# Kernel optimization log

Hardware: AMD Instinct MI355X
Metric: run time of the kernel (lower is better)

## Reference

```python
import jax, jax.numpy as jnp
import numpy as np

B, H, S, DK = 4, 16, 2048, 64
NEG_INF = -1e9


def setup_inputs() -> dict:
    key = jax.random.key(0)
    kq, kk, kv, ks = jax.random.split(key, 4)
    q = jax.random.normal(kq, (B, H, S, DK), dtype=jnp.float32)
    k = jax.random.normal(kk, (B, H, S, DK), dtype=jnp.float32)
    v = jax.random.normal(kv, (B, H, S, DK), dtype=jnp.float32)
    # valid lengths in [S//2, S] so no row is fully masked (causal + padding)
    sen_len = jax.random.randint(ks, (B,), S // 2, S + 1, dtype=jnp.int64)
    return {"q": q, "k": k, "v": v, "sen_len": sen_len}


def reference(q, k, v, sen_len):
    # att = q @ k^T / sqrt(d_k)   -> (B, H, S, S)
    att = jnp.einsum("bhqd,bhkd->bhqk", q, k) / np.sqrt(DK).astype(np.float32)
    pos = jnp.arange(S)
    # causal (ahead) mask: query i may not attend to key j > i
    causal = pos[None, :] > pos[:, None]                      # (S, S)
    # padding mask: key positions >= sen_len[b] are invalid
    pad = pos[None, :] >= sen_len[:, None]                    # (B, S)
    mask = causal[None, None, :, :] | pad[:, None, None, :]   # (B, 1, S, S) broadcast over H
    att = jnp.where(mask, jnp.float32(NEG_INF), att)
    att = jax.nn.softmax(att, axis=-1)
    return jnp.einsum("bhqk,bhkd->bhqd", att, v)
```

## Files before the change

### kernel.cpp

```cpp
#include <hip/hip_runtime.h>
#include <hip/hip_bf16.h>

#define B_   4
#define H_   16
#define S_   2048
#define DK_  64
#define NBH  64
#define QSCALE (0.125f * 1.44269504f)

typedef __attribute__((ext_vector_type(8)))  short    short8;
typedef __attribute__((ext_vector_type(4)))  float    f32x4;
typedef __attribute__((ext_vector_type(16))) float    f32x16;
typedef __attribute__((ext_vector_type(4)))  unsigned u32x4;

__device__ __forceinline__ unsigned short f2bf(float f) {
    union { float f; unsigned int u; } x; x.f = f;
    unsigned int r = x.u + 0x7fffu + ((x.u >> 16) & 1u);
    return (unsigned short)(r >> 16);
}

__device__ __forceinline__ unsigned cvtpk(float a, float b) {
    unsigned r;
    asm("v_cvt_pk_bf16_f32 %0, %1, %2" : "=v"(r) : "v"(a), "v"(b));
    return r;
}
__device__ __forceinline__ void pl32swap(unsigned& a, unsigned& b) {
    asm("v_permlane32_swap_b32 %0, %1" : "+v"(a), "+v"(b));
}

__global__ __launch_bounds__(256) void conv_k(const float* __restrict__ in,
                                              unsigned short* __restrict__ out) {
    const long i = (long)(blockIdx.x * 256 + threadIdx.x) * 8;
    const float4* p = (const float4*)(in + i);
    float4 a = p[0], b = p[1];
    short8 f;
    f[0] = (short)f2bf(a.x); f[1] = (short)f2bf(a.y);
    f[2] = (short)f2bf(a.z); f[3] = (short)f2bf(a.w);
    f[4] = (short)f2bf(b.x); f[5] = (short)f2bf(b.y);
    f[6] = (short)f2bf(b.z); f[7] = (short)f2bf(b.w);
    *(short8*)(out + i) = f;
}

__global__ __launch_bounds__(256) void transp_v(const float* __restrict__ v,
                                                unsigned short* __restrict__ vt) {
    const int s0 = blockIdx.x * 64;
    const int bh = blockIdx.y;
    const int s  = threadIdx.x & 63;
    const int dq = threadIdx.x >> 6;
    const float* src = v + ((long)bh * S_ + s0 + s) * DK_;
    unsigned short* dst = vt + (long)bh * DK_ * S_ + s0 + s;
    #pragma unroll
    for (int j4 = 0; j4 < 4; ++j4) {
        const int d4 = dq * 16 + j4 * 4;
        float4 a = *(const float4*)(src + d4);
        dst[(long)(d4 + 0) * S_] = f2bf(a.x);
        dst[(long)(d4 + 1) * S_] = f2bf(a.y);
        dst[(long)(d4 + 2) * S_] = f2bf(a.z);
        dst[(long)(d4 + 3) * S_] = f2bf(a.w);
    }
}

template <bool PRECONV>
__global__ __launch_bounds__(256, 2) void attn_fwd3(
    const float* __restrict__ q, const float* __restrict__ k32,
    const float* __restrict__ v32, const unsigned short* __restrict__ kbf,
    const unsigned short* __restrict__ vtbf, const int* __restrict__ sen_len,
    float* __restrict__ out)
{
    const int qt = (S_ / 128 - 1) - blockIdx.x;
    const int bh = blockIdx.y;
    const int b  = bh >> 4;
    const int q0 = qt * 128;
    const long base = (long)bh * S_ * DK_;

    const int tid  = threadIdx.x;
    const int wid  = tid >> 6;
    const int lane = tid & 63;
    const int l31  = lane & 31;
    const int hi   = lane >> 5;

    __shared__ unsigned short Klds[64 * 64];
    __shared__ unsigned short Vlds[64 * 64];
    char* const KldsB = (char*)Klds;
    char* const VldsB = (char*)Vlds;

    const int slen = sen_len[b];
    const int q0w  = q0 + wid * 32;
    const int iq   = q0w + l31;

    short8 qf[4];
    {
        const float* qp = q + base + (long)iq * DK_ + hi * 8;
        #pragma unroll
        for (int ks = 0; ks < 4; ++ks) {
            float4 a = *(const float4*)(qp + ks * 16);
            float4 c = *(const float4*)(qp + ks * 16 + 4);
            short8 f;
            f[0] = (short)f2bf(a.x * QSCALE); f[1] = (short)f2bf(a.y * QSCALE);
            f[2] = (short)f2bf(a.z * QSCALE); f[3] = (short)f2bf(a.w * QSCALE);
            f[4] = (short)f2bf(c.x * QSCALE); f[5] = (short)f2bf(c.y * QSCALE);
            f[6] = (short)f2bf(c.z * QSCALE); f[7] = (short)f2bf(c.w * QSCALE);
            qf[ks] = f;
        }
    }

    f32x16 O0 = (f32x16)(0.f), O1 = (f32x16)(0.f);
    float m_ = -INFINITY, l_ = 0.f;

    const int nk     = min(q0 + 128, slen);
    const int ntiles = (nk + 63) >> 6;
    const int wmax   = q0w + 31;

    for (int t = 0; t < ntiles; ++t) {
        const int k0 = t * 64;

        if (PRECONV) {
            const unsigned short* ksrc = kbf + base + (long)k0 * DK_;
            const unsigned short* vsrc = vtbf + (long)bh * DK_ * S_ + k0;
            #pragma unroll
            for (int it = 0; it < 2; ++it) {
                const int c = tid + 256 * it;
                const int r = c >> 3, slot = c & 7;
                const int dst = r * 128 + ((slot * 16) ^ ((r & 7) << 4));
                *(short8*)(KldsB + dst) = *(const short8*)(ksrc + r * DK_ + slot * 8);
                *(short8*)(VldsB + dst) = *(const short8*)(vsrc + (long)r * S_ + slot * 8);
            }
        } else {
            const float* ks32 = k32 + base + (long)k0 * DK_;
            #pragma unroll
            for (int it = 0; it < 2; ++it) {
                const int c = tid + 256 * it;
                const int r = c >> 3, slot = c & 7;
                const float4* p = (const float4*)(ks32 + r * DK_ + slot * 8);
                float4 a = p[0], bq = p[1];
                short8 f;
                f[0] = (short)f2bf(a.x);  f[1] = (short)f2bf(a.y);
                f[2] = (short)f2bf(a.z);  f[3] = (short)f2bf(a.w);
                f[4] = (short)f2bf(bq.x); f[5] = (short)f2bf(bq.y);
                f[6] = (short)f2bf(bq.z); f[7] = (short)f2bf(bq.w);
                *(short8*)(KldsB + r * 128 + ((slot * 16) ^ ((r & 7) << 4))) = f;
            }
            const float* vs32 = v32 + base + (long)k0 * DK_;
            #pragma unroll
            for (int it = 0; it < 4; ++it) {
                const int c = tid + 256 * it;
                const int s = c >> 4, d4 = (c & 15) * 4;
                float4 a = *(const float4*)(vs32 + s * DK_ + d4);
                unsigned short vals[4] = {f2bf(a.x), f2bf(a.y), f2bf(a.z), f2bf(a.w)};
                #pragma unroll
                for (int j = 0; j < 4; ++j)
                    *(unsigned short*)(VldsB + (d4 + j) * 128 +
                                       ((2 * s) ^ (((d4 + j) & 7) << 4))) = vals[j];
            }
        }
        __syncthreads();

        if (k0 <= wmax) {
            f32x16 s0 = (f32x16)(0.f), s1 = (f32x16)(0.f);
            #pragma unroll
            for (int ks = 0; ks < 4; ++ks) {
                const int col = ks * 32 + hi * 16;
                const int r0 = l31, r1 = 32 + l31;
                short8 kf0 = *(const short8*)(KldsB + r0 * 128 + (col ^ ((r0 & 7) << 4)));
                short8 kf1 = *(const short8*)(KldsB + r1 * 128 + (col ^ ((r1 & 7) << 4)));
                s0 = __builtin_amdgcn_mfma_f32_32x32x16_bf16(kf0, qf[ks], s0, 0, 0, 0);
                s1 = __builtin_amdgcn_mfma_f32_32x32x16_bf16(kf1, qf[ks], s1, 0, 0, 0);
            }

            if (!((k0 + 63 <= q0w) && (k0 + 63 < slen))) {
                #pragma unroll
                for (int r = 0; r < 16; ++r) {
                    const int joff = k0 + (r & 3) + 8 * (r >> 2) + 4 * hi;
                    const int j0 = joff, j1 = joff + 32;
                    if (!((j0 <= iq) && (j0 < slen))) s0[r] = -1e30f;
                    if (!((j1 <= iq) && (j1 < slen))) s1[r] = -1e30f;
                }
            }

            float pm = s0[0];
            #pragma unroll
            for (int r = 1; r < 16; ++r) pm = fmaxf(pm, s0[r]);
            #pragma unroll
            for (int r = 0; r < 16; ++r) pm = fmaxf(pm, s1[r]);
            pm = fmaxf(pm, __shfl_xor(pm, 32, 64));
            const float mnew = fmaxf(m_, pm);
            const float resc = exp2f(m_ - mnew);
            m_ = mnew;
            float rs = 0.f;
            #pragma unroll
            for (int r = 0; r < 16; ++r) { s0[r] = exp2f(s0[r] - mnew); rs += s0[r]; }
            #pragma unroll
            for (int r = 0; r < 16; ++r) { s1[r] = exp2f(s1[r] - mnew); rs += s1[r]; }
            rs += __shfl_xor(rs, 32, 64);
            l_ = l_ * resc + rs;
            O0 *= resc;
            O1 *= resc;

            u32x4 pw[4];
            {
                unsigned a0 = cvtpk(s0[0], s0[1]),  c0 = cvtpk(s0[2], s0[3]);
                unsigned b0 = cvtpk(s0[4], s0[5]),  d0 = cvtpk(s0[6], s0[7]);
                pl32swap(a0, b0); pl32swap(c0, d0);
                pw[0] = (u32x4){a0, c0, b0, d0};
                unsigned a1 = cvtpk(s0[8], s0[9]),  c1 = cvtpk(s0[10], s0[11]);
                unsigned b1 = cvtpk(s0[12], s0[13]), d1 = cvtpk(s0[14], s0[15]);
                pl32swap(a1, b1); pl32swap(c1, d1);
                pw[1] = (u32x4){a1, c1, b1, d1};
                unsigned a2 = cvtpk(s1[0], s1[1]),  c2 = cvtpk(s1[2], s1[3]);
                unsigned b2 = cvtpk(s1[4], s1[5]),  d2 = cvtpk(s1[6], s1[7]);
                pl32swap(a2, b2); pl32swap(c2, d2);
                pw[2] = (u32x4){a2, c2, b2, d2};
                unsigned a3 = cvtpk(s1[8], s1[9]),  c3 = cvtpk(s1[10], s1[11]);
                unsigned b3 = cvtpk(s1[12], s1[13]), d3 = cvtpk(s1[14], s1[15]);
                pl32swap(a3, b3); pl32swap(c3, d3);
                pw[3] = (u32x4){a3, c3, b3, d3};
            }

            #pragma unroll
            for (int s = 0; s < 4; ++s) {
                short8 pf = __builtin_bit_cast(short8, pw[s]);
                const int col = s * 32 + hi * 16;
                const int r0 = l31, r1 = 32 + l31;
                short8 vf0 = *(const short8*)(VldsB + r0 * 128 + (col ^ ((r0 & 7) << 4)));
                short8 vf1 = *(const short8*)(VldsB + r1 * 128 + (col ^ ((r1 & 7) << 4)));
                O0 = __builtin_amdgcn_mfma_f32_32x32x16_bf16(vf0, pf, O0, 0, 0, 0);
                O1 = __builtin_amdgcn_mfma_f32_32x32x16_bf16(vf1, pf, O1, 0, 0, 0);
            }
        }
        __syncthreads();
    }

    const float inv = 1.0f / l_;
    float* op = out + base + (long)iq * DK_;
    #pragma unroll
    for (int rq = 0; rq < 4; ++rq) {
        float4 f0, f1;
        f0.x = O0[rq * 4 + 0] * inv; f0.y = O0[rq * 4 + 1] * inv;
        f0.z = O0[rq * 4 + 2] * inv; f0.w = O0[rq * 4 + 3] * inv;
        f1.x = O1[rq * 4 + 0] * inv; f1.y = O1[rq * 4 + 1] * inv;
        f1.z = O1[rq * 4 + 2] * inv; f1.w = O1[rq * 4 + 3] * inv;
        *(float4*)(op + rq * 8 + hi * 4)      = f0;
        *(float4*)(op + 32 + rq * 8 + hi * 4) = f1;
    }
}

extern "C" void kernel_launch(void* const* d_in, const int* in_sizes, int n_in,
                              void* d_out, int out_size, void* d_ws, size_t ws_size,
                              hipStream_t stream) {
    const float* q = (const float*)d_in[0];
    const float* k = (const float*)d_in[1];
    const float* v = (const float*)d_in[2];
    const int* sen_len = (const int*)d_in[3];
    float* out = (float*)d_out;

    const size_t kv_elems = (size_t)NBH * S_ * DK_;
    const bool pre = ws_size >= kv_elems * 2 * sizeof(unsigned short);
    unsigned short* kbf  = (unsigned short*)d_ws;
    unsigned short* vtbf = kbf + kv_elems;

    if (pre) {
        conv_k<<<dim3((unsigned)(kv_elems / 2048)), dim3(256), 0, stream>>>(k, kbf);
        transp_v<<<dim3(S_ / 64, NBH), dim3(256), 0, stream>>>(v, vtbf);
        attn_fwd3<true><<<dim3(S_ / 128, NBH), dim3(256), 0, stream>>>(
            q, k, v, kbf, vtbf, sen_len, out);
    } else {
        attn_fwd3<false><<<dim3(S_ / 128, NBH), dim3(256), 0, stream>>>(
            q, k, v, kbf, vtbf, sen_len, out);
    }
}
```

Measured before the change: 229.7 us.

## Double-buffer K/V tiles in LDS with register prefetch and lazy softmax rescale

K/V tiles now live in two LDS buffers. The next tile is loaded into registers before the current tile's MFMA work and written to the other buffer afterwards, which leaves one barrier per tile instead of two. The change also raises the launch-bounds occupancy hint to 4 blocks, adds s_setprio around the MFMA sections, and uses a tree max reduction. The running max is now rescaled only when the new max exceeds the old by more than 8, which skips most O rescales. The costs are higher register pressure from the prefetch registers under a tighter register budget, plus a slightly different numeric path for the softmax.

Result: slower. 238.2 us (+3.7%).

```diff
diff --git a/kernel.cpp b/kernel.cpp
--- a/kernel.cpp
+++ b/kernel.cpp
@@ -9,7 +9,6 @@
 #define QSCALE (0.125f * 1.44269504f)
 
 typedef __attribute__((ext_vector_type(8)))  short    short8;
-typedef __attribute__((ext_vector_type(4)))  float    f32x4;
 typedef __attribute__((ext_vector_type(16))) float    f32x16;
 typedef __attribute__((ext_vector_type(4)))  unsigned u32x4;
 
@@ -18,7 +17,6 @@
     unsigned int r = x.u + 0x7fffu + ((x.u >> 16) & 1u);
     return (unsigned short)(r >> 16);
 }
-
 __device__ __forceinline__ unsigned cvtpk(float a, float b) {
     unsigned r;
     asm("v_cvt_pk_bf16_f32 %0, %1, %2" : "=v"(r) : "v"(a), "v"(b));
@@ -61,7 +59,7 @@
 }
 
 template <bool PRECONV>
-__global__ __launch_bounds__(256, 2) void attn_fwd3(
+__global__ __launch_bounds__(256, 4) void attn_fwd4(
     const float* __restrict__ q, const float* __restrict__ k32,
     const float* __restrict__ v32, const unsigned short* __restrict__ kbf,
     const unsigned short* __restrict__ vtbf, const int* __restrict__ sen_len,
@@ -71,7 +69,8 @@
     const int bh = blockIdx.y;
     const int b  = bh >> 4;
     const int q0 = qt * 128;
-    const long base = (long)bh * S_ * DK_;
+    const long base   = (long)bh * S_ * DK_;
+    const long vtbase = (long)bh * DK_ * S_;
 
     const int tid  = threadIdx.x;
     const int wid  = tid >> 6;
@@ -79,10 +78,8 @@
     const int l31  = lane & 31;
     const int hi   = lane >> 5;
 
-    __shared__ unsigned short Klds[64 * 64];
-    __shared__ unsigned short Vlds[64 * 64];
-    char* const KldsB = (char*)Klds;
-    char* const VldsB = (char*)Vlds;
+    __shared__ unsigned short Klds[2][64 * 64];
+    __shared__ unsigned short Vlds[2][64 * 64];
 
     const int slen = sen_len[b];
     const int q0w  = q0 + wid * 32;
@@ -111,90 +108,130 @@
     const int ntiles = (nk + 63) >> 6;
     const int wmax   = q0w + 31;
 
+    if (PRECONV) {
+        const unsigned short* ksrc = kbf + base;
+        const unsigned short* vsrc = vtbf + vtbase;
+        #pragma unroll
+        for (int it = 0; it < 2; ++it) {
+            const int c = tid + 256 * it, r = c >> 3, slot = c & 7;
+            const int dst = r * 128 + ((slot * 16) ^ ((r & 7) << 4));
+            *(short8*)((char*)Klds[0] + dst) = *(const short8*)(ksrc + r * DK_ + slot * 8);
+            *(short8*)((char*)Vlds[0] + dst) = *(const short8*)(vsrc + (long)r * S_ + slot * 8);
+        }
+    } else {
+        const float* ks32 = k32 + base;
+        #pragma unroll
+        for (int it = 0; it < 2; ++it) {
+            const int c = tid + 256 * it, r = c >> 3, slot = c & 7;
+            const float4* p = (const float4*)(ks32 + r * DK_ + slot * 8);
+            float4 a = p[0], bq = p[1];
+            short8 f;
+            f[0] = (short)f2bf(a.x);  f[1] = (short)f2bf(a.y);
+            f[2] = (short)f2bf(a.z);  f[3] = (short)f2bf(a.w);
+            f[4] = (short)f2bf(bq.x); f[5] = (short)f2bf(bq.y);
+            f[6] = (short)f2bf(bq.z); f[7] = (short)f2bf(bq.w);
+            *(short8*)((char*)Klds[0] + r * 128 + ((slot * 16) ^ ((r & 7) << 4))) = f;
+        }
+        const float* vs32 = v32 + base;
+        #pragma unroll
+        for (int it = 0; it < 4; ++it) {
+            const int c = tid + 256 * it, s = c >> 4, d4 = (c & 15) * 4;
+            float4 a = *(const float4*)(vs32 + s * DK_ + d4);
+            unsigned short vals[4] = {f2bf(a.x), f2bf(a.y), f2bf(a.z), f2bf(a.w)};
+            #pragma unroll
+            for (int j = 0; j < 4; ++j)
+                *(unsigned short*)((char*)Vlds[0] + (d4 + j) * 128 +
+                                   ((2 * s) ^ (((d4 + j) & 7) << 4))) = vals[j];
+        }
+    }
+    __syncthreads();
+
+    int cur = 0;
     for (int t = 0; t < ntiles; ++t) {
         const int k0 = t * 64;
-
-        if (PRECONV) {
-            const unsigned short* ksrc = kbf + base + (long)k0 * DK_;
-            const unsigned short* vsrc = vtbf + (long)bh * DK_ * S_ + k0;
-            #pragma unroll
-            for (int it = 0; it < 2; ++it) {
-                const int c = tid + 256 * it;
-                const int r = c >> 3, slot = c & 7;
-                const int dst = r * 128 + ((slot * 16) ^ ((r & 7) << 4));
-                *(short8*)(KldsB + dst) = *(const short8*)(ksrc + r * DK_ + slot * 8);
-                *(short8*)(VldsB + dst) = *(const short8*)(vsrc + (long)r * S_ + slot * 8);
-            }
-        } else {
-            const float* ks32 = k32 + base + (long)k0 * DK_;
-            #pragma unroll
-            for (int it = 0; it < 2; ++it) {
-                const int c = tid + 256 * it;
-                const int r = c >> 3, slot = c & 7;
-                const float4* p = (const float4*)(ks32 + r * DK_ + slot * 8);
-                float4 a = p[0], bq = p[1];
-                short8 f;
-                f[0] = (short)f2bf(a.x);  f[1] = (short)f2bf(a.y);
-                f[2] = (short)f2bf(a.z);  f[3] = (short)f2bf(a.w);
-                f[4] = (short)f2bf(bq.x); f[5] = (short)f2bf(bq.y);
-                f[6] = (short)f2bf(bq.z); f[7] = (short)f2bf(bq.w);
-                *(short8*)(KldsB + r * 128 + ((slot * 16) ^ ((r & 7) << 4))) = f;
-            }
-            const float* vs32 = v32 + base + (long)k0 * DK_;
-            #pragma unroll
-            for (int it = 0; it < 4; ++it) {
-                const int c = tid + 256 * it;
-                const int s = c >> 4, d4 = (c & 15) * 4;
-                float4 a = *(const float4*)(vs32 + s * DK_ + d4);
-                unsigned short vals[4] = {f2bf(a.x), f2bf(a.y), f2bf(a.z), f2bf(a.w)};
-                #pragma unroll
-                for (int j = 0; j < 4; ++j)
-                    *(unsigned short*)(VldsB + (d4 + j) * 128 +
-                                       ((2 * s) ^ (((d4 + j) & 7) << 4))) = vals[j];
-            }
-        }
-        __syncthreads();
+        const bool more = (t + 1 < ntiles);
+
+        short8 kst[2], vst[2];
+        float4 kr[2][2], vr[4];
+        if (more) {
+            if (PRECONV) {
+                const unsigned short* ksrc = kbf + base + (long)(k0 + 64) * DK_;
+                const unsigned short* vsrc = vtbf + vtbase + (k0 + 64);
+                #pragma unroll
+                for (int it = 0; it < 2; ++it) {
+                    const int c = tid + 256 * it, r = c >> 3, slot = c & 7;
+                    kst[it] = *(const short8*)(ksrc + r * DK_ + slot * 8);
+                    vst[it] = *(const short8*)(vsrc + (long)r * S_ + slot * 8);
+                }
+            } else {
+                const float* ks32 = k32 + base + (long)(k0 + 64) * DK_;
+                #pragma unroll
+                for (int it = 0; it < 2; ++it) {
+                    const int c = tid + 256 * it, r = c >> 3, slot = c & 7;
+                    kr[it][0] = *(const float4*)(ks32 + r * DK_ + slot * 8);
+                    kr[it][1] = *(const float4*)(ks32 + r * DK_ + slot * 8 + 4);
+                }
+                const float* vs32 = v32 + base + (long)(k0 + 64) * DK_;
+                #pragma unroll
+                for (int it = 0; it < 4; ++it) {
+                    const int c = tid + 256 * it, s = c >> 4, d4 = (c & 15) * 4;
+                    vr[it] = *(const float4*)(vs32 + s * DK_ + d4);
+                }
+            }
+        }
+        __builtin_amdgcn_sched_barrier(0);
 
         if (k0 <= wmax) {
+            const char* KB = (const char*)Klds[cur];
+            const char* VB = (const char*)Vlds[cur];
+            const int sw = (l31 & 7) << 4;
+            const int rb = l31 * 128;
+
             f32x16 s0 = (f32x16)(0.f), s1 = (f32x16)(0.f);
+            __builtin_amdgcn_s_setprio(1);
             #pragma unroll
             for (int ks = 0; ks < 4; ++ks) {
-                const int col = ks * 32 + hi * 16;
-                const int r0 = l31, r1 = 32 + l31;
-                short8 kf0 = *(const short8*)(KldsB + r0 * 128 + (col ^ ((r0 & 7) << 4)));
-                short8 kf1 = *(const short8*)(KldsB + r1 * 128 + (col ^ ((r1 & 7) << 4)));
+                const int col = (ks * 32 + hi * 16) ^ sw;
+                short8 kf0 = *(const short8*)(KB + rb + col);
+                short8 kf1 = *(const short8*)(KB + 4096 + rb + col);
                 s0 = __builtin_amdgcn_mfma_f32_32x32x16_bf16(kf0, qf[ks], s0, 0, 0, 0);
                 s1 = __builtin_amdgcn_mfma_f32_32x32x16_bf16(kf1, qf[ks], s1, 0, 0, 0);
             }
+            __builtin_amdgcn_s_setprio(0);
 
             if (!((k0 + 63 <= q0w) && (k0 + 63 < slen))) {
                 #pragma unroll
                 for (int r = 0; r < 16; ++r) {
                     const int joff = k0 + (r & 3) + 8 * (r >> 2) + 4 * hi;
-                    const int j0 = joff, j1 = joff + 32;
-                    if (!((j0 <= iq) && (j0 < slen))) s0[r] = -1e30f;
-                    if (!((j1 <= iq) && (j1 < slen))) s1[r] = -1e30f;
-                }
-            }
-
-            float pm = s0[0];
-            #pragma unroll
-            for (int r = 1; r < 16; ++r) pm = fmaxf(pm, s0[r]);
-            #pragma unroll
-            for (int r = 0; r < 16; ++r) pm = fmaxf(pm, s1[r]);
+                    if (!((joff <= iq) && (joff < slen))) s0[r] = -1e30f;
+                    if (!((joff + 32 <= iq) && (joff + 32 < slen))) s1[r] = -1e30f;
+                }
+            }
+
+            float x[16];
+            #pragma unroll
+            for (int i = 0; i < 16; ++i) x[i] = fmaxf(s0[i], s1[i]);
+            #pragma unroll
+            for (int st = 8; st >= 1; st >>= 1)
+                #pragma unroll
+                for (int i = 0; i < 8; ++i)
+                    if (i < st) x[i] = fmaxf(x[i], x[i + st]);
+            float pm = x[0];
             pm = fmaxf(pm, __shfl_xor(pm, 32, 64));
-            const float mnew = fmaxf(m_, pm);
-            const float resc = exp2f(m_ - mnew);
-            m_ = mnew;
-            float rs = 0.f;
-            #pragma unroll
-            for (int r = 0; r < 16; ++r) { s0[r] = exp2f(s0[r] - mnew); rs += s0[r]; }
-            #pragma unroll
-            for (int r = 0; r < 16; ++r) { s1[r] = exp2f(s1[r] - mnew); rs += s1[r]; }
-            rs += __shfl_xor(rs, 32, 64);
-            l_ = l_ * resc + rs;
-            O0 *= resc;
-            O1 *= resc;
+            if (!__all(pm <= m_ + 8.0f)) {
+                const float mn = fmaxf(m_, pm);
+                const float rc = exp2f(m_ - mn);
+                m_ = mn; l_ *= rc;
+                O0 *= rc; O1 *= rc;
+            }
+            float rs[4] = {0.f, 0.f, 0.f, 0.f};
+            #pragma unroll
+            for (int i = 0; i < 16; ++i) { s0[i] = exp2f(s0[i] - m_); rs[i & 3] += s0[i]; }
+            #pragma unroll
+            for (int i = 0; i < 16; ++i) { s1[i] = exp2f(s1[i] - m_); rs[i & 3] += s1[i]; }
+            float rsum = (rs[0] + rs[1]) + (rs[2] + rs[3]);
+            rsum += __shfl_xor(rsum, 32, 64);
+            l_ += rsum;
 
             u32x4 pw[4];
             {
@@ -202,7 +239,7 @@
                 unsigned b0 = cvtpk(s0[4], s0[5]),  d0 = cvtpk(s0[6], s0[7]);
                 pl32swap(a0, b0); pl32swap(c0, d0);
                 pw[0] = (u32x4){a0, c0, b0, d0};
-                unsigned a1 = cvtpk(s0[8], s0[9]),  c1 = cvtpk(s0[10], s0[11]);
+                unsigned a1 = cvtpk(s0[8], s0[9]),   c1 = cvtpk(s0[10], s0[11]);
                 unsigned b1 = cvtpk(s0[12], s0[13]), d1 = cvtpk(s0[14], s0[15]);
                 pl32swap(a1, b1); pl32swap(c1, d1);
                 pw[1] = (u32x4){a1, c1, b1, d1};
@@ -210,24 +247,63 @@
                 unsigned b2 = cvtpk(s1[4], s1[5]),  d2 = cvtpk(s1[6], s1[7]);
                 pl32swap(a2, b2); pl32swap(c2, d2);
                 pw[2] = (u32x4){a2, c2, b2, d2};
-                unsigned a3 = cvtpk(s1[8], s1[9]),  c3 = cvtpk(s1[10], s1[11]);
+                unsigned a3 = cvtpk(s1[8], s1[9]),   c3 = cvtpk(s1[10], s1[11]);
                 unsigned b3 = cvtpk(s1[12], s1[13]), d3 = cvtpk(s1[14], s1[15]);
                 pl32swap(a3, b3); pl32swap(c3, d3);
                 pw[3] = (u32x4){a3, c3, b3, d3};
             }
 
+            __builtin_amdgcn_s_setprio(1);
             #pragma unroll
             for (int s = 0; s < 4; ++s) {
                 short8 pf = __builtin_bit_cast(short8, pw[s]);
-                const int col = s * 32 + hi * 16;
-                const int r0 = l31, r1 = 32 + l31;
-                short8 vf0 = *(const short8*)(VldsB + r0 * 128 + (col ^ ((r0 & 7) << 4)));
-                short8 vf1 = *(const short8*)(VldsB + r1 * 128 + (col ^ ((r1 & 7) << 4)));
+                const int col = (s * 32 + hi * 16) ^ sw;
+                short8 vf0 = *(const short8*)(VB + rb + col);
+                short8 vf1 = *(const short8*)(VB + 4096 + rb + col);
                 O0 = __builtin_amdgcn_mfma_f32_32x32x16_bf16(vf0, pf, O0, 0, 0, 0);
                 O1 = __builtin_amdgcn_mfma_f32_32x32x16_bf16(vf1, pf, O1, 0, 0, 0);
             }
-        }
-        __syncthreads();
+            __builtin_amdgcn_s_setprio(0);
+        }
+        __builtin_amdgcn_sched_barrier(0);
+
+        if (more) {
+            char* KB = (char*)Klds[cur ^ 1];
+            char* VB = (char*)Vlds[cur ^ 1];
+            if (PRECONV) {
+                #pragma unroll
+                for (int it = 0; it < 2; ++it) {
+                    const int c = tid + 256 * it, r = c >> 3, slot = c & 7;
+                    const int dst = r * 128 + ((slot * 16) ^ ((r & 7) << 4));
+                    *(short8*)(KB + dst) = kst[it];
+                    *(short8*)(VB + dst) = vst[it];
+                }
+            } else {
+                #pragma unroll
+                for (int it = 0; it < 2; ++it) {
+                    const int c = tid + 256 * it, r = c >> 3, slot = c & 7;
+                    float4 a = kr[it][0], bq = kr[it][1];
+                    short8 f;
+                    f[0] = (short)f2bf(a.x);  f[1] = (short)f2bf(a.y);
+                    f[2] = (short)f2bf(a.z);  f[3] = (short)f2bf(a.w);
+                    f[4] = (short)f2bf(bq.x); f[5] = (short)f2bf(bq.y);
+                    f[6] = (short)f2bf(bq.z); f[7] = (short)f2bf(bq.w);
+                    *(short8*)(KB + r * 128 + ((slot * 16) ^ ((r & 7) << 4))) = f;
+                }
+                #pragma unroll
+                for (int it = 0; it < 4; ++it) {
+                    const int c = tid + 256 * it, s = c >> 4, d4 = (c & 15) * 4;
+                    float4 a = vr[it];
+                    unsigned short vals[4] = {f2bf(a.x), f2bf(a.y), f2bf(a.z), f2bf(a.w)};
+                    #pragma unroll
+                    for (int j = 0; j < 4; ++j)
+                        *(unsigned short*)(VB + (d4 + j) * 128 +
+                                           ((2 * s) ^ (((d4 + j) & 7) << 4))) = vals[j];
+                }
+            }
+            __syncthreads();
+        }
+        cur ^= 1;
     }
 
     const float inv = 1.0f / l_;
@@ -261,10 +337,10 @@
     if (pre) {
         conv_k<<<dim3((unsigned)(kv_elems / 2048)), dim3(256), 0, stream>>>(k, kbf);
         transp_v<<<dim3(S_ / 64, NBH), dim3(256), 0, stream>>>(v, vtbf);
-        attn_fwd3<true><<<dim3(S_ / 128, NBH), dim3(256), 0, stream>>>(
+        attn_fwd4<true><<<dim3(S_ / 128, NBH), dim3(256), 0, stream>>>(
             q, k, v, kbf, vtbf, sen_len, out);
     } else {
-        attn_fwd3<false><<<dim3(S_ / 128, NBH), dim3(256), 0, stream>>>(
+        attn_fwd4<false><<<dim3(S_ / 128, NBH), dim3(256), 0, stream>>>(
             q, k, v, kbf, vtbf, sen_len, out);
     }
 }
```
